# Kernel tuning notes

Measured on AMD Instinct MI355X. Metric: run time of the kernel, lower is better.

Reference implementation:

```python
import jax, jax.numpy as jnp
import numpy as np

WS = 8          # window size
HEADS = 3       # num_heads
DIM = 48        # channels


def _rel_pos_log(ws):
    # log-spaced relative coordinates, (N, N, 2) with N = ws*ws
    coords = jnp.stack(jnp.meshgrid(jnp.arange(ws), jnp.arange(ws), indexing='ij'))  # (2, ws, ws)
    cf = coords.reshape(2, -1)                                  # (2, N)
    rel = (cf[:, :, None] - cf[:, None, :]).transpose(1, 2, 0)  # (N, N, 2)
    rel = rel.astype(jnp.float32)
    return jnp.sign(rel) * jnp.log1p(jnp.abs(rel))


def setup_inputs() -> dict:
    key = jax.random.key(0)
    ks = jax.random.split(key, 11)
    s = 0.05  # keep pre-softmax logits in a sane range
    return {
        'X': jax.random.normal(ks[0], (2, DIM, 512, 512), jnp.float32),
        'v_w': jax.random.normal(ks[1], (DIM, DIM), jnp.float32) * s,
        'v_b': jnp.zeros((DIM,), jnp.float32),
        'qk_w': jax.random.normal(ks[2], (2 * DIM, DIM), jnp.float32) * s,
        'qk_b': jnp.zeros((2 * DIM,), jnp.float32),
        'proj_w': jax.random.normal(ks[3], (DIM, DIM), jnp.float32) * s,
        'proj_b': jnp.zeros((DIM,), jnp.float32),
        'meta1_w': jax.random.normal(ks[4], (256, 2), jnp.float32) * s,
        'meta1_b': jnp.zeros((256,), jnp.float32),
        'meta2_w': jax.random.normal(ks[5], (HEADS, 256), jnp.float32) * s,
        'meta2_b': jnp.zeros((HEADS,), jnp.float32),
    }


def _conv1x1(x, w, b):
    # x: [B, Cin, H, W], w: [Cout, Cin], b: [Cout]
    return jnp.einsum('oc,bchw->bohw', w, x) + b[None, :, None, None]


def reference(X, v_w, v_b, qk_w, qk_b, proj_w, proj_b,
              meta1_w, meta1_b, meta2_w, meta2_b):
    B, C, H, W = X.shape
    hd = C // HEADS
    scale = hd ** -0.5
    N = WS * WS

    V = _conv1x1(X, v_w, v_b)              # [B, C, H, W]
    QK = _conv1x1(X, qk_w, qk_b)           # [B, 2C, H, W]
    QKV = jnp.concatenate([QK, V], axis=1)  # [B, 3C, H, W]

    # window partition (shift=0, H/W multiples of WS -> no padding)
    nh, nw = H // WS, W // WS
    x = QKV.transpose(0, 2, 3, 1)                           # [B, H, W, 3C]
    x = x.reshape(B, nh, WS, nw, WS, 3 * C)
    x = x.transpose(0, 1, 3, 2, 4, 5).reshape(B * nh * nw, N, 3 * C)

    qkv = x.reshape(-1, N, 3, HEADS, hd).transpose(2, 0, 3, 1, 4)  # [3, B_, h, N, d]
    q, k, v = qkv[0], qkv[1], qkv[2]

    attn = jnp.einsum('bhnd,bhmd->bhnm', q * scale, k)       # [B_, h, N, N]

    # MLP relative position bias
    rel = _rel_pos_log(WS)                                   # [N, N, 2]
    hidden = jax.nn.relu(rel @ meta1_w.T + meta1_b)          # [N, N, 256]
    bias = (hidden @ meta2_w.T + meta2_b).transpose(2, 0, 1)  # [h, N, N]

    attn = jax.nn.softmax(attn + bias[None], axis=-1)
    out = jnp.einsum('bhnm,bhmd->bhnd', attn, v)             # [B_, h, N, d]
    out = out.transpose(0, 2, 1, 3).reshape(B * nh * nw, N, C)

    # window reverse
    out = out.reshape(B, nh, nw, WS, WS, C)
    out = out.transpose(0, 1, 3, 2, 4, 5).reshape(B, H, W, C)
    out = out.transpose(0, 3, 1, 2)                          # [B, C, H, W]

    return _conv1x1(out, proj_w, proj_b)
```

## Files before the change

kernel.cpp:

```cpp
#include <hip/hip_runtime.h>
#include <math.h>


typedef _Float16 f16x4 __attribute__((ext_vector_type(4)));
typedef float    f32x4 __attribute__((ext_vector_type(4)));

#define LOG2E 1.44269504f

#define WS_BFRAG 0
#define WS_WFRAG 49152
#define WS_PFRAG 62976
#define WS_QKVB  67584
#define WS_PBIAS 68160

#define XT_S 52
#define T_S  100
#define VD_S 68

__global__ __launch_bounds__(256) void prep_kernel(
    const float* __restrict__ m1w, const float* __restrict__ m1b,
    const float* __restrict__ m2w, const float* __restrict__ m2b,
    const float* __restrict__ qk_w, const float* __restrict__ v_w,
    const float* __restrict__ proj_w,
    const float* __restrict__ qk_b, const float* __restrict__ v_b,
    const float* __restrict__ proj_b,
    unsigned char* __restrict__ ws)
{
    __shared__ float sm[1536];

    float*     bfrag = (float*)(ws + WS_BFRAG);
    _Float16*  wfrag = (_Float16*)(ws + WS_WFRAG);
    _Float16*  pfrag = (_Float16*)(ws + WS_PFRAG);
    float*     qkvb  = (float*)(ws + WS_QKVB);
    float*     pbias = (float*)(ws + WS_PBIAS);

    const int gid = blockIdx.x * 256 + threadIdx.x;
    if (blockIdx.x < 16) {
        for (int i = threadIdx.x; i < 1536; i += 256) {
            float v;
            if (i < 512)      v = m1w[i];
            else if (i < 768) v = m1b[i - 512];
            else              v = m2w[i - 768];
            sm[i] = v;
        }
        __syncthreads();

        const int n = gid >> 6, m = gid & 63;
        float di = (float)((n >> 3) - (m >> 3));
        float dj = (float)((n & 7) - (m & 7));
        float r0 = copysignf(log1pf(fabsf(di)), di);
        float r1 = copysignf(log1pf(fabsf(dj)), dj);
        float a0 = 0.f, a1 = 0.f, a2 = 0.f;
        #pragma unroll 4
        for (int k = 0; k < 256; ++k) {
            float hv = fmaxf(sm[512 + k] + sm[2*k]*r0 + sm[2*k+1]*r1, 0.f);
            a0 += sm[768 + k]  * hv;
            a1 += sm[1024 + k] * hv;
            a2 += sm[1280 + k] * hv;
        }
        const int tm = m >> 4, quad = (m >> 2) & 3, r = m & 3, tn = n >> 4;
        const int ln = quad*16 + (n & 15);
        const int base = ((tm*4 + tn)*64 + ln)*4 + r;
        bfrag[(0*16*64)*4  + base] = (a0 + m2b[0]) * LOG2E;
        bfrag[(16*64)*4    + base] = (a1 + m2b[1]) * LOG2E;
        bfrag[(32*64)*4    + base] = (a2 + m2b[2]) * LOG2E;
    } else if (gid < 4096 + 6912) {
        const int idx = gid - 4096;
        const int j = idx & 3, l = (idx >> 2) & 63, f = idx >> 8;
        const int ks = f % 3, mt = f / 3;
        const int row = mt*16 + (l & 15), col = ks*16 + ((l >> 4) << 2) + j;
        const float wv = (row < 96) ? qk_w[row*48 + col] : v_w[(row-96)*48 + col];
        wfrag[idx] = (_Float16)wv;
    } else if (gid < 11008 + 2304) {
        const int idx = gid - 11008;
        const int j = idx & 3, l = (idx >> 2) & 63, f = idx >> 8;
        const int ks = f % 3, mt = f / 3;
        const int row = mt*16 + (l & 15), col = ks*16 + ((l >> 4) << 2) + j;
        pfrag[idx] = (_Float16)proj_w[row*48 + col];
    } else if (gid < 13312 + 144) {
        const int c = gid - 13312;
        qkvb[c] = (c < 96) ? qk_b[c] : v_b[c - 96];
    } else if (gid < 13456 + 48) {
        pbias[gid - 13456] = proj_b[gid - 13456];
    }
}

__global__ __launch_bounds__(256, 4) void win_attn_kernel(
    const float* __restrict__ X, const unsigned char* __restrict__ ws,
    float* __restrict__ out, int nblk)
{
    __shared__ _Float16 smem[12992];
    _Float16* sXO = smem;
    _Float16* sT  = smem + 64*XT_S;
    _Float16* sVd = smem + 64*XT_S + 64*T_S;

    const float* bfrag = (const float*)(ws + WS_BFRAG);
    const f16x4* wfrag = (const f16x4*)(ws + WS_WFRAG);
    const f16x4* pfrag = (const f16x4*)(ws + WS_PFRAG);
    const float* qkvb  = (const float*)(ws + WS_QKVB);
    const float* pbias = (const float*)(ws + WS_PBIAS);

    const int tid  = threadIdx.x;
    const int wave = tid >> 6, lane = tid & 63;
    const int lq   = lane >> 4, lm = lane & 15;

    const int blk = blockIdx.x;
    const int wid = (blk & 7) * (nblk >> 3) + (blk >> 3);
    const int batch = wid >> 12;
    const int wh = (wid >> 6) & 63, ww = wid & 63;
    const int h0 = wh << 3, w0 = ww << 3;

    const float* Xb = X + ((size_t)batch * 48 << 18);

    {
        const int tok = lane;
        const size_t pix = (size_t)(h0 + (tok >> 3)) * 512 + (w0 + (tok & 7));
        #pragma unroll
        for (int k = 0; k < 12; ++k) {
            const int c = wave + (k << 2);
            sXO[tok*XT_S + c] = (_Float16)Xb[((size_t)c << 18) + pix];
        }
    }
    __syncthreads();

    {
        f16x4 bx[3];
        #pragma unroll
        for (int ks = 0; ks < 3; ++ks)
            bx[ks] = *(const f16x4*)&sXO[(wave*16 + lm)*XT_S + ks*16 + lq*4];
        f16x4 aw[27];
        #pragma unroll
        for (int f = 0; f < 27; ++f) aw[f] = wfrag[f*64 + lane];

        const int tok = wave*16 + lm;
        #pragma unroll
        for (int mt = 0; mt < 9; ++mt) {
            f32x4 acc = *(const f32x4*)&qkvb[mt*16 + lq*4];
            #pragma unroll
            for (int ks = 0; ks < 3; ++ks)
                acc = __builtin_amdgcn_mfma_f32_16x16x16f16(aw[mt*3+ks], bx[ks], acc, 0, 0, 0);
            if (mt < 3) {
                f16x4 hv;
                #pragma unroll
                for (int r = 0; r < 4; ++r) hv[r] = (_Float16)(acc[r] * (0.25f * LOG2E));
                *(f16x4*)&sT[tok*T_S + mt*16 + lq*4] = hv;
            } else if (mt < 6) {
                f16x4 hv;
                #pragma unroll
                for (int r = 0; r < 4; ++r) hv[r] = (_Float16)acc[r];
                *(f16x4*)&sT[tok*T_S + mt*16 + lq*4] = hv;
            } else {
                #pragma unroll
                for (int r = 0; r < 4; ++r)
                    sVd[((mt-6)*16 + lq*4 + r)*VD_S + tok] = (_Float16)acc[r];
            }
        }
    }
    __syncthreads();

    if (wave < 3) {
        const int h = wave;
        f16x4 ak[4], bq[4];
        #pragma unroll
        for (int t = 0; t < 4; ++t) {
            ak[t] = *(const f16x4*)&sT[(t*16 + lm)*T_S + 48 + h*16 + lq*4];
            bq[t] = *(const f16x4*)&sT[(t*16 + lm)*T_S + h*16 + lq*4];
        }
        f32x4 s[4][4];
        const f32x4* bf = (const f32x4*)bfrag + (size_t)h*16*64;
        #pragma unroll
        for (int tm = 0; tm < 4; ++tm)
            #pragma unroll
            for (int tn = 0; tn < 4; ++tn) {
                f32x4 c = bf[(tm*4 + tn)*64 + lane];
                s[tm][tn] = __builtin_amdgcn_mfma_f32_16x16x16f16(ak[tm], bq[tn], c, 0, 0, 0);
            }
        float rinv[4];
        #pragma unroll
        for (int tn = 0; tn < 4; ++tn) {
            float sum = 0.f;
            #pragma unroll
            for (int tm = 0; tm < 4; ++tm)
                #pragma unroll
                for (int r = 0; r < 4; ++r) {
                    float e = __builtin_amdgcn_exp2f(s[tm][tn][r]);
                    s[tm][tn][r] = e; sum += e;
                }
            sum += __shfl_xor(sum, 16);
            sum += __shfl_xor(sum, 32);
            rinv[tn] = __builtin_amdgcn_rcpf(sum);
        }
        f16x4 av[4];
        #pragma unroll
        for (int tm = 0; tm < 4; ++tm)
            av[tm] = *(const f16x4*)&sVd[(h*16 + lm)*VD_S + tm*16 + lq*4];
        #pragma unroll
        for (int tn = 0; tn < 4; ++tn) {
            f32x4 o = {0.f, 0.f, 0.f, 0.f};
            #pragma unroll
            for (int tm = 0; tm < 4; ++tm) {
                f16x4 pf;
                pf[0] = (_Float16)s[tm][tn][0];
                pf[1] = (_Float16)s[tm][tn][1];
                pf[2] = (_Float16)s[tm][tn][2];
                pf[3] = (_Float16)s[tm][tn][3];
                o = __builtin_amdgcn_mfma_f32_16x16x16f16(av[tm], pf, o, 0, 0, 0);
            }
            f16x4 hv;
            #pragma unroll
            for (int r = 0; r < 4; ++r) hv[r] = (_Float16)(o[r] * rinv[tn]);
            *(f16x4*)&sXO[(tn*16 + lm)*XT_S + h*16 + lq*4] = hv;
        }
    }
    __syncthreads();

    {
        f16x4 bo[3];
        #pragma unroll
        for (int ks = 0; ks < 3; ++ks)
            bo[ks] = *(const f16x4*)&sXO[(wave*16 + lm)*XT_S + ks*16 + lq*4];
        f16x4 ap[9];
        #pragma unroll
        for (int f = 0; f < 9; ++f) ap[f] = pfrag[f*64 + lane];

        const int tok = wave*16 + lm;
        float* ob = out + ((size_t)batch * 48 << 18);
        const size_t pix = (size_t)(h0 + (tok >> 3)) * 512 + (w0 + (tok & 7));
        #pragma unroll
        for (int mt = 0; mt < 3; ++mt) {
            f32x4 acc = *(const f32x4*)&pbias[mt*16 + lq*4];
            #pragma unroll
            for (int ks = 0; ks < 3; ++ks)
                acc = __builtin_amdgcn_mfma_f32_16x16x16f16(ap[mt*3+ks], bo[ks], acc, 0, 0, 0);
            #pragma unroll
            for (int r = 0; r < 4; ++r)
                ob[((size_t)(mt*16 + lq*4 + r) << 18) + pix] = acc[r];
        }
    }
}

extern "C" void kernel_launch(void* const* d_in, const int* in_sizes, int n_in,
                              void* d_out, int out_size, void* d_ws, size_t ws_size,
                              hipStream_t stream) {
    (void)n_in; (void)out_size; (void)ws_size;
    const float* X      = (const float*)d_in[0];
    const float* v_w    = (const float*)d_in[1];
    const float* v_b    = (const float*)d_in[2];
    const float* qk_w   = (const float*)d_in[3];
    const float* qk_b   = (const float*)d_in[4];
    const float* proj_w = (const float*)d_in[5];
    const float* proj_b = (const float*)d_in[6];
    const float* m1w    = (const float*)d_in[7];
    const float* m1b    = (const float*)d_in[8];
    const float* m2w    = (const float*)d_in[9];
    const float* m2b    = (const float*)d_in[10];
    float* out = (float*)d_out;
    unsigned char* ws = (unsigned char*)d_ws;

    const int B = in_sizes[0] / (48 * 512 * 512);
    const int nblk = B * 64 * 64;

    hipLaunchKernelGGL(prep_kernel, dim3(53), dim3(256), 0, stream,
                       m1w, m1b, m2w, m2b, qk_w, v_w, proj_w, qk_b, v_b, proj_b, ws);
    hipLaunchKernelGGL(win_attn_kernel, dim3(nblk), dim3(256), 0, stream,
                       X, ws, out, nblk);
}
```

Baseline: 259.8 us.

## Process two adjacent windows per block with register-prefetched input

Each block now handles two horizontally adjacent 8x8 windows instead of one, halving the grid size. While the first window is being computed, the second window's X values are prefetched from global memory into registers, so load latency overlaps with MFMA work. This adds 12 registers per thread and an extra barrier, which may cut occupancy or leave less parallelism to hide latency.

```diff
diff --git a/kernel.cpp b/kernel.cpp
--- a/kernel.cpp
+++ b/kernel.cpp
@@ -87,7 +87,7 @@
 
 __global__ __launch_bounds__(256, 4) void win_attn_kernel(
     const float* __restrict__ X, const unsigned char* __restrict__ ws,
-    float* __restrict__ out, int nblk)
+    float* __restrict__ out, int npair)
 {
     __shared__ _Float16 smem[12992];
     _Float16* sXO = smem;
@@ -104,137 +104,156 @@
     const int wave = tid >> 6, lane = tid & 63;
     const int lq   = lane >> 4, lm = lane & 15;
 
-    const int blk = blockIdx.x;
-    const int wid = (blk & 7) * (nblk >> 3) + (blk >> 3);
-    const int batch = wid >> 12;
-    const int wh = (wid >> 6) & 63, ww = wid & 63;
-    const int h0 = wh << 3, w0 = ww << 3;
+    const int b = blockIdx.x;
+    const int pair = (b & 7) * (npair >> 3) + (b >> 3);
+    const int wid0 = pair << 1;
+    const int batch = wid0 >> 12;
+    const int wh = (wid0 >> 6) & 63, ww0 = wid0 & 63;
+    const int h0 = wh << 3;
 
     const float* Xb = X + ((size_t)batch * 48 << 18);
-
-    {
-        const int tok = lane;
-        const size_t pix = (size_t)(h0 + (tok >> 3)) * 512 + (w0 + (tok & 7));
+    float*       ob = out + ((size_t)batch * 48 << 18);
+
+    const int tok = lane;
+    const size_t pixbase = (size_t)(h0 + (tok >> 3)) * 512 + (tok & 7);
+
+    float xc[12];
+    #pragma unroll
+    for (int k = 0; k < 12; ++k) {
+        const int c = wave + (k << 2);
+        xc[k] = Xb[((size_t)c << 18) + pixbase + (ww0 << 3)];
+    }
+
+    #pragma unroll 1
+    for (int w = 0; w < 2; ++w) {
+        const int w0 = (ww0 + w) << 3;
+        if (w) __syncthreads();
+
         #pragma unroll
-        for (int k = 0; k < 12; ++k) {
-            const int c = wave + (k << 2);
-            sXO[tok*XT_S + c] = (_Float16)Xb[((size_t)c << 18) + pix];
-        }
-    }
-    __syncthreads();
-
-    {
-        f16x4 bx[3];
-        #pragma unroll
-        for (int ks = 0; ks < 3; ++ks)
-            bx[ks] = *(const f16x4*)&sXO[(wave*16 + lm)*XT_S + ks*16 + lq*4];
-        f16x4 aw[27];
-        #pragma unroll
-        for (int f = 0; f < 27; ++f) aw[f] = wfrag[f*64 + lane];
-
-        const int tok = wave*16 + lm;
-        #pragma unroll
-        for (int mt = 0; mt < 9; ++mt) {
-            f32x4 acc = *(const f32x4*)&qkvb[mt*16 + lq*4];
+        for (int k = 0; k < 12; ++k)
+            sXO[tok*XT_S + wave + (k << 2)] = (_Float16)xc[k];
+        __syncthreads();
+
+        if (w == 0) {
+            #pragma unroll
+            for (int k = 0; k < 12; ++k) {
+                const int c = wave + (k << 2);
+                xc[k] = Xb[((size_t)c << 18) + pixbase + ((ww0 + 1) << 3)];
+            }
+        }
+
+        {
+            f16x4 bx[3];
             #pragma unroll
             for (int ks = 0; ks < 3; ++ks)
-                acc = __builtin_amdgcn_mfma_f32_16x16x16f16(aw[mt*3+ks], bx[ks], acc, 0, 0, 0);
-            if (mt < 3) {
+                bx[ks] = *(const f16x4*)&sXO[(wave*16 + lm)*XT_S + ks*16 + lq*4];
+            f16x4 aw[27];
+            #pragma unroll
+            for (int f = 0; f < 27; ++f) aw[f] = wfrag[f*64 + lane];
+
+            const int tk = wave*16 + lm;
+            #pragma unroll
+            for (int mt = 0; mt < 9; ++mt) {
+                f32x4 acc = *(const f32x4*)&qkvb[mt*16 + lq*4];
+                #pragma unroll
+                for (int ks = 0; ks < 3; ++ks)
+                    acc = __builtin_amdgcn_mfma_f32_16x16x16f16(aw[mt*3+ks], bx[ks], acc, 0, 0, 0);
+                if (mt < 3) {
+                    f16x4 hv;
+                    #pragma unroll
+                    for (int r = 0; r < 4; ++r) hv[r] = (_Float16)(acc[r] * (0.25f * LOG2E));
+                    *(f16x4*)&sT[tk*T_S + mt*16 + lq*4] = hv;
+                } else if (mt < 6) {
+                    f16x4 hv;
+                    #pragma unroll
+                    for (int r = 0; r < 4; ++r) hv[r] = (_Float16)acc[r];
+                    *(f16x4*)&sT[tk*T_S + mt*16 + lq*4] = hv;
+                } else {
+                    #pragma unroll
+                    for (int r = 0; r < 4; ++r)
+                        sVd[((mt-6)*16 + lq*4 + r)*VD_S + tk] = (_Float16)acc[r];
+                }
+            }
+        }
+        __syncthreads();
+
+        if (wave < 3) {
+            const int h = wave;
+            f16x4 ak[4], bq[4];
+            #pragma unroll
+            for (int t = 0; t < 4; ++t) {
+                ak[t] = *(const f16x4*)&sT[(t*16 + lm)*T_S + 48 + h*16 + lq*4];
+                bq[t] = *(const f16x4*)&sT[(t*16 + lm)*T_S + h*16 + lq*4];
+            }
+            f32x4 s[4][4];
+            const f32x4* bf = (const f32x4*)bfrag + (size_t)h*16*64;
+            #pragma unroll
+            for (int tm = 0; tm < 4; ++tm)
+                #pragma unroll
+                for (int tn = 0; tn < 4; ++tn) {
+                    f32x4 c = bf[(tm*4 + tn)*64 + lane];
+                    s[tm][tn] = __builtin_amdgcn_mfma_f32_16x16x16f16(ak[tm], bq[tn], c, 0, 0, 0);
+                }
+            float rinv[4];
+            #pragma unroll
+            for (int tn = 0; tn < 4; ++tn) {
+                float sum = 0.f;
+                #pragma unroll
+                for (int tm = 0; tm < 4; ++tm)
+                    #pragma unroll
+                    for (int r = 0; r < 4; ++r) {
+                        float e = __builtin_amdgcn_exp2f(s[tm][tn][r]);
+                        s[tm][tn][r] = e; sum += e;
+                    }
+                sum += __shfl_xor(sum, 16);
+                sum += __shfl_xor(sum, 32);
+                rinv[tn] = __builtin_amdgcn_rcpf(sum);
+            }
+            f16x4 av[4];
+            #pragma unroll
+            for (int tm = 0; tm < 4; ++tm)
+                av[tm] = *(const f16x4*)&sVd[(h*16 + lm)*VD_S + tm*16 + lq*4];
+            #pragma unroll
+            for (int tn = 0; tn < 4; ++tn) {
+                f32x4 o = {0.f, 0.f, 0.f, 0.f};
+                #pragma unroll
+                for (int tm = 0; tm < 4; ++tm) {
+                    f16x4 pf;
+                    pf[0] = (_Float16)s[tm][tn][0];
+                    pf[1] = (_Float16)s[tm][tn][1];
+                    pf[2] = (_Float16)s[tm][tn][2];
+                    pf[3] = (_Float16)s[tm][tn][3];
+                    o = __builtin_amdgcn_mfma_f32_16x16x16f16(av[tm], pf, o, 0, 0, 0);
+                }
                 f16x4 hv;
                 #pragma unroll
-                for (int r = 0; r < 4; ++r) hv[r] = (_Float16)(acc[r] * (0.25f * LOG2E));
-                *(f16x4*)&sT[tok*T_S + mt*16 + lq*4] = hv;
-            } else if (mt < 6) {
-                f16x4 hv;
-                #pragma unroll
-                for (int r = 0; r < 4; ++r) hv[r] = (_Float16)acc[r];
-                *(f16x4*)&sT[tok*T_S + mt*16 + lq*4] = hv;
-            } else {
+                for (int r = 0; r < 4; ++r) hv[r] = (_Float16)(o[r] * rinv[tn]);
+                *(f16x4*)&sXO[(tn*16 + lm)*XT_S + h*16 + lq*4] = hv;
+            }
+        }
+        __syncthreads();
+
+        {
+            f16x4 bo[3];
+            #pragma unroll
+            for (int ks = 0; ks < 3; ++ks)
+                bo[ks] = *(const f16x4*)&sXO[(wave*16 + lm)*XT_S + ks*16 + lq*4];
+            f16x4 ap[9];
+            #pragma unroll
+            for (int f = 0; f < 9; ++f) ap[f] = pfrag[f*64 + lane];
+
+            const int tk = wave*16 + lm;
+            const size_t pix = (size_t)(h0 + (tk >> 3)) * 512 + (w0 + (tk & 7));
+            #pragma unroll
+            for (int mt = 0; mt < 3; ++mt) {
+                f32x4 acc = *(const f32x4*)&pbias[mt*16 + lq*4];
+                #pragma unroll
+                for (int ks = 0; ks < 3; ++ks)
+                    acc = __builtin_amdgcn_mfma_f32_16x16x16f16(ap[mt*3+ks], bo[ks], acc, 0, 0, 0);
                 #pragma unroll
                 for (int r = 0; r < 4; ++r)
-                    sVd[((mt-6)*16 + lq*4 + r)*VD_S + tok] = (_Float16)acc[r];
-            }
-        }
-    }
-    __syncthreads();
-
-    if (wave < 3) {
-        const int h = wave;
-        f16x4 ak[4], bq[4];
-        #pragma unroll
-        for (int t = 0; t < 4; ++t) {
-            ak[t] = *(const f16x4*)&sT[(t*16 + lm)*T_S + 48 + h*16 + lq*4];
-            bq[t] = *(const f16x4*)&sT[(t*16 + lm)*T_S + h*16 + lq*4];
-        }
-        f32x4 s[4][4];
-        const f32x4* bf = (const f32x4*)bfrag + (size_t)h*16*64;
-        #pragma unroll
-        for (int tm = 0; tm < 4; ++tm)
-            #pragma unroll
-            for (int tn = 0; tn < 4; ++tn) {
-                f32x4 c = bf[(tm*4 + tn)*64 + lane];
-                s[tm][tn] = __builtin_amdgcn_mfma_f32_16x16x16f16(ak[tm], bq[tn], c, 0, 0, 0);
-            }
-        float rinv[4];
-        #pragma unroll
-        for (int tn = 0; tn < 4; ++tn) {
-            float sum = 0.f;
-            #pragma unroll
-            for (int tm = 0; tm < 4; ++tm)
-                #pragma unroll
-                for (int r = 0; r < 4; ++r) {
-                    float e = __builtin_amdgcn_exp2f(s[tm][tn][r]);
-                    s[tm][tn][r] = e; sum += e;
-                }
-            sum += __shfl_xor(sum, 16);
-            sum += __shfl_xor(sum, 32);
-            rinv[tn] = __builtin_amdgcn_rcpf(sum);
-        }
-        f16x4 av[4];
-        #pragma unroll
-        for (int tm = 0; tm < 4; ++tm)
-            av[tm] = *(const f16x4*)&sVd[(h*16 + lm)*VD_S + tm*16 + lq*4];
-        #pragma unroll
-        for (int tn = 0; tn < 4; ++tn) {
-            f32x4 o = {0.f, 0.f, 0.f, 0.f};
-            #pragma unroll
-            for (int tm = 0; tm < 4; ++tm) {
-                f16x4 pf;
-                pf[0] = (_Float16)s[tm][tn][0];
-                pf[1] = (_Float16)s[tm][tn][1];
-                pf[2] = (_Float16)s[tm][tn][2];
-                pf[3] = (_Float16)s[tm][tn][3];
-                o = __builtin_amdgcn_mfma_f32_16x16x16f16(av[tm], pf, o, 0, 0, 0);
-            }
-            f16x4 hv;
-            #pragma unroll
-            for (int r = 0; r < 4; ++r) hv[r] = (_Float16)(o[r] * rinv[tn]);
-            *(f16x4*)&sXO[(tn*16 + lm)*XT_S + h*16 + lq*4] = hv;
-        }
-    }
-    __syncthreads();
-
-    {
-        f16x4 bo[3];
-        #pragma unroll
-        for (int ks = 0; ks < 3; ++ks)
-            bo[ks] = *(const f16x4*)&sXO[(wave*16 + lm)*XT_S + ks*16 + lq*4];
-        f16x4 ap[9];
-        #pragma unroll
-        for (int f = 0; f < 9; ++f) ap[f] = pfrag[f*64 + lane];
-
-        const int tok = wave*16 + lm;
-        float* ob = out + ((size_t)batch * 48 << 18);
-        const size_t pix = (size_t)(h0 + (tok >> 3)) * 512 + (w0 + (tok & 7));
-        #pragma unroll
-        for (int mt = 0; mt < 3; ++mt) {
-            f32x4 acc = *(const f32x4*)&pbias[mt*16 + lq*4];
-            #pragma unroll
-            for (int ks = 0; ks < 3; ++ks)
-                acc = __builtin_amdgcn_mfma_f32_16x16x16f16(ap[mt*3+ks], bo[ks], acc, 0, 0, 0);
-            #pragma unroll
-            for (int r = 0; r < 4; ++r)
-                ob[((size_t)(mt*16 + lq*4 + r) << 18) + pix] = acc[r];
+                    ob[((size_t)(mt*16 + lq*4 + r) << 18) + pix] = acc[r];
+            }
         }
     }
 }
@@ -258,10 +277,10 @@
     unsigned char* ws = (unsigned char*)d_ws;
 
     const int B = in_sizes[0] / (48 * 512 * 512);
-    const int nblk = B * 64 * 64;
+    const int npair = B * 64 * 32;
 
     hipLaunchKernelGGL(prep_kernel, dim3(53), dim3(256), 0, stream,
                        m1w, m1b, m2w, m2b, qk_w, v_w, proj_w, qk_b, v_b, proj_b, ws);
-    hipLaunchKernelGGL(win_attn_kernel, dim3(nblk), dim3(256), 0, stream,
-                       X, ws, out, nblk);
+    hipLaunchKernelGGL(win_attn_kernel, dim3(npair), dim3(256), 0, stream,
+                       X, ws, out, npair);
 }
```

Measured after the change: 564.3 us. 117% more time.
